# Performance work log

Measured on AMD Instinct MI355X. Metric: run time of the kernel, lower is better.

Reference implementation:

```python
import jax, jax.numpy as jnp
import numpy as np

N_POINTS = 200000   # number of voxels
N_CLUSTS = 4096     # number of clusters
P = 64              # points per cluster (regularized fixed size)
E = 32768           # number of (directed) edges


def setup_inputs() -> dict:
    key = jax.random.key(0)
    k1, k2, k3 = jax.random.split(key, 3)
    data = jax.random.normal(k1, (N_POINTS, 4), dtype=jnp.float32)
    clusts = jax.random.randint(k2, (N_CLUSTS, P), 0, N_POINTS, dtype=jnp.int64)
    edge_index = jax.random.randint(k3, (2, E), 0, N_CLUSTS, dtype=jnp.int64)
    return {"data": data, "clusts": clusts, "edge_index": edge_index}


def reference(data, clusts, edge_index):
    coords = data[:, 1:4]                      # [N, 3] voxel coordinates
    c1 = clusts[edge_index[0]]                 # [E, P] point indices of source cluster
    c2 = clusts[edge_index[1]]                 # [E, P] point indices of target cluster
    x1 = coords[c1]                            # [E, P, 3]
    x2 = coords[c2]                            # [E, P, 3]
    e, p = c1.shape
    # pairwise squared distances per edge: [E, P, P]
    d2 = jnp.sum((x1[:, :, None, :] - x2[:, None, :, :]) ** 2, axis=-1)
    imin = jnp.argmin(d2.reshape(e, p * p), axis=1)   # flat argmin of closest pair
    i1 = imin // p
    i2 = imin % p
    v1 = jnp.take_along_axis(x1, i1[:, None, None], axis=1)[:, 0, :]  # [E, 3]
    v2 = jnp.take_along_axis(x2, i2[:, None, None], axis=1)[:, 0, :]  # [E, 3]
    disp = v1 - v2                                                    # [E, 3]
    lend = jnp.linalg.norm(disp, axis=1, keepdims=True)               # [E, 1]
    safe = jnp.where(lend > 0, lend, jnp.ones_like(lend))
    disp = jnp.where(lend > 0, disp / safe, disp)                     # unit displacement
    B = (disp[:, :, None] * disp[:, None, :]).reshape(e, 9)           # outer product, flat
    return jnp.concatenate([v1, v2, disp, lend, B], axis=1)           # [E, 19]
```

## Files before the change

### kernel.cpp

```cpp
#include <hip/hip_runtime.h>

#ifndef FLT_MAX
#define FLT_MAX 3.402823466e+38f
#endif

__device__ __forceinline__ float rlanef(float v, int j) {
    return __uint_as_float(__builtin_amdgcn_readlane(__float_as_uint(v), j));
}

__device__ __forceinline__ float sel3(int i, float a, float b, float c) {
    return i == 0 ? a : (i == 1 ? b : c);
}

__device__ __forceinline__ float d2f(float ax, float ay, float az,
                                     float bx, float by, float bz) {
    const float dx = __fsub_rn(ax, bx);
    const float dy = __fsub_rn(ay, by);
    const float dz = __fsub_rn(az, bz);
    return __builtin_fmaf(dx, dx, __builtin_fmaf(dy, dy, __fmul_rn(dz, dz)));
}

__global__ __launch_bounds__(256, 8) void clustgeo_edge_kernel(
    const float* __restrict__ data,
    const int*   __restrict__ clusts,
    const int*   __restrict__ eidx,
    float*       __restrict__ out,
    int E)
{
    const int wave = threadIdx.x >> 6;
    const int lane = threadIdx.x & 63;
    const int e = blockIdx.x * 4 + wave;
    if (e >= E) return;

    __shared__ float sx2[4][3][64];

    const int a = eidx[e];
    const int b = eidx[E + e];
    const int p1 = clusts[a * 64 + lane];
    const int p2 = clusts[b * 64 + lane];
    const float4 r1 = *reinterpret_cast<const float4*>(data + (size_t)p1 * 4);
    const float4 r2 = *reinterpret_cast<const float4*>(data + (size_t)p2 * 4);
    const float x1x = r1.y, x1y = r1.z, x1z = r1.w;
    const float x2x = r2.y, x2y = r2.z, x2z = r2.w;
    sx2[wave][0][lane] = x2x;
    sx2[wave][1][lane] = x2y;
    sx2[wave][2][lane] = x2z;

    const float4* rx = reinterpret_cast<const float4*>(&sx2[wave][0][0]);
    const float4* ry = reinterpret_cast<const float4*>(&sx2[wave][1][0]);
    const float4* rz = reinterpret_cast<const float4*>(&sx2[wave][2][0]);

    float b0 = FLT_MAX, b1 = FLT_MAX, b2 = FLT_MAX, b3 = FLT_MAX;
    #pragma unroll 4
    for (int g = 0; g < 16; ++g) {
        const float4 X = rx[g];
        const float4 Y = ry[g];
        const float4 Z = rz[g];
        b0 = fminf(b0, d2f(x1x, x1y, x1z, X.x, Y.x, Z.x));
        b1 = fminf(b1, d2f(x1x, x1y, x1z, X.y, Y.y, Z.y));
        b2 = fminf(b2, d2f(x1x, x1y, x1z, X.z, Y.z, Z.z));
        b3 = fminf(b3, d2f(x1x, x1y, x1z, X.w, Y.w, Z.w));
    }
    const float rowmin = fminf(fminf(b0, b1), fminf(b2, b3));

    float bm = rowmin;
    #pragma unroll
    for (int off = 32; off; off >>= 1) bm = fminf(bm, __shfl_xor(bm, off, 64));

    const unsigned long long mi = __ballot(rowmin == bm);
    const int i1 = (int)__ffsll(mi) - 1;

    const float v1x = rlanef(x1x, i1);
    const float v1y = rlanef(x1y, i1);
    const float v1z = rlanef(x1z, i1);
    const float dj = d2f(v1x, v1y, v1z, x2x, x2y, x2z);
    const unsigned long long mj = __ballot(dj == bm);
    const int i2 = (int)__ffsll(mj) - 1;

    const float v2x = rlanef(x2x, i2);
    const float v2y = rlanef(x2y, i2);
    const float v2z = rlanef(x2z, i2);

    float dx = v1x - v2x, dy = v1y - v2y, dz = v1z - v2z;
    const float lend = sqrtf(dx * dx + dy * dy + dz * dz);
    if (lend > 0.f) { dx /= lend; dy /= lend; dz /= lend; }

    if (lane < 19) {
        float o;
        if (lane < 3)       o = sel3(lane,     v1x, v1y, v1z);
        else if (lane < 6)  o = sel3(lane - 3, v2x, v2y, v2z);
        else if (lane < 9)  o = sel3(lane - 6, dx, dy, dz);
        else if (lane == 9) o = lend;
        else {
            const int k = lane - 10;
            o = sel3(k / 3, dx, dy, dz) * sel3(k % 3, dx, dy, dz);
        }
        out[(size_t)e * 19 + lane] = o;
    }
}

extern "C" void kernel_launch(void* const* d_in, const int* in_sizes, int n_in,
                              void* d_out, int out_size, void* d_ws, size_t ws_size,
                              hipStream_t stream) {
    const float* data   = (const float*)d_in[0];
    const int*   clusts = (const int*)d_in[1];
    const int*   eidx   = (const int*)d_in[2];
    float*       out    = (float*)d_out;
    const int E = in_sizes[2] / 2;
    const int blocks = (E + 3) / 4;
    clustgeo_edge_kernel<<<blocks, 256, 0, stream>>>(data, clusts, eidx, out, E);
}
```

Measured before the change: 33.71 us.

## Process two edges per wave with half-wave split and packed fp32 math

Each 64-lane wave now handles two edges: each half-wave owns one edge, and each lane holds two source points (rows) instead of one. The pairwise distance loop uses 2-wide float vectors so the compiler can emit packed FMA/min instructions, and it reuses each LDS read across two rows. The reductions, ballots and readlanes are split per half-wave, and the grid is halved. This is meant to cut per-edge overhead from index loads, reductions and launch, at the cost of more registers per thread and more complex lane-selection logic.

```diff
diff --git a/kernel.cpp b/kernel.cpp
--- a/kernel.cpp
+++ b/kernel.cpp
@@ -4,8 +4,11 @@
 #define FLT_MAX 3.402823466e+38f
 #endif
 
-__device__ __forceinline__ float rlanef(float v, int j) {
-    return __uint_as_float(__builtin_amdgcn_readlane(__float_as_uint(v), j));
+typedef float v2f __attribute__((ext_vector_type(2)));
+typedef float v4f __attribute__((ext_vector_type(4)));
+
+__device__ __forceinline__ float rlanef(float v, int l) {
+    return __uint_as_float(__builtin_amdgcn_readlane(__float_as_uint(v), l));
 }
 
 __device__ __forceinline__ float sel3(int i, float a, float b, float c) {
@@ -29,73 +32,126 @@
 {
     const int wave = threadIdx.x >> 6;
     const int lane = threadIdx.x & 63;
-    const int e = blockIdx.x * 4 + wave;
-    if (e >= E) return;
+    const int hl   = lane & 31;
+    const bool hiH = lane >= 32;
+    const int e  = blockIdx.x * 8 + wave * 2 + (hiH ? 1 : 0);
+    const int ec = e < E ? e : (E - 1);
 
-    __shared__ float sx2[4][3][64];
+    __shared__ __align__(16) float sx2[4][2][3][64];
 
-    const int a = eidx[e];
-    const int b = eidx[E + e];
-    const int p1 = clusts[a * 64 + lane];
-    const int p2 = clusts[b * 64 + lane];
-    const float4 r1 = *reinterpret_cast<const float4*>(data + (size_t)p1 * 4);
-    const float4 r2 = *reinterpret_cast<const float4*>(data + (size_t)p2 * 4);
-    const float x1x = r1.y, x1y = r1.z, x1z = r1.w;
-    const float x2x = r2.y, x2y = r2.z, x2z = r2.w;
-    sx2[wave][0][lane] = x2x;
-    sx2[wave][1][lane] = x2y;
-    sx2[wave][2][lane] = x2z;
+    const int ca = eidx[ec];
+    const int cb = eidx[E + ec];
+    const int p1a = clusts[ca * 64 + hl];
+    const int p1b = clusts[ca * 64 + hl + 32];
+    const int p2a = clusts[cb * 64 + hl];
+    const int p2b = clusts[cb * 64 + hl + 32];
+    const float4 q1a = *reinterpret_cast<const float4*>(data + (size_t)p1a * 4);
+    const float4 q1b = *reinterpret_cast<const float4*>(data + (size_t)p1b * 4);
+    const float4 q2a = *reinterpret_cast<const float4*>(data + (size_t)p2a * 4);
+    const float4 q2b = *reinterpret_cast<const float4*>(data + (size_t)p2b * 4);
+    const float x1ax=q1a.y, x1ay=q1a.z, x1az=q1a.w;
+    const float x1bx=q1b.y, x1by=q1b.z, x1bz=q1b.w;
+    const float x2ax=q2a.y, x2ay=q2a.z, x2az=q2a.w;
+    const float x2bx=q2b.y, x2by=q2b.z, x2bz=q2b.w;
 
-    const float4* rx = reinterpret_cast<const float4*>(&sx2[wave][0][0]);
-    const float4* ry = reinterpret_cast<const float4*>(&sx2[wave][1][0]);
-    const float4* rz = reinterpret_cast<const float4*>(&sx2[wave][2][0]);
+    float* hbase = &sx2[wave][hiH ? 1 : 0][0][0];
+    hbase[hl      ] = x2ax;  hbase[hl + 32      ] = x2bx;
+    hbase[hl + 64 ] = x2ay;  hbase[hl + 32 + 64 ] = x2by;
+    hbase[hl + 128] = x2az;  hbase[hl + 32 + 128] = x2bz;
 
-    float b0 = FLT_MAX, b1 = FLT_MAX, b2 = FLT_MAX, b3 = FLT_MAX;
-    #pragma unroll 4
+    const v2f xA = {x1ax, x1ax}, yA = {x1ay, x1ay}, zA = {x1az, x1az};
+    const v2f xB = {x1bx, x1bx}, yB = {x1by, x1by}, zB = {x1bz, x1bz};
+
+    v2f r0c01 = {FLT_MAX, FLT_MAX}, r0c23 = {FLT_MAX, FLT_MAX};
+    v2f r1c01 = {FLT_MAX, FLT_MAX}, r1c23 = {FLT_MAX, FLT_MAX};
+    #pragma unroll 2
     for (int g = 0; g < 16; ++g) {
-        const float4 X = rx[g];
-        const float4 Y = ry[g];
-        const float4 Z = rz[g];
-        b0 = fminf(b0, d2f(x1x, x1y, x1z, X.x, Y.x, Z.x));
-        b1 = fminf(b1, d2f(x1x, x1y, x1z, X.y, Y.y, Z.y));
-        b2 = fminf(b2, d2f(x1x, x1y, x1z, X.z, Y.z, Z.z));
-        b3 = fminf(b3, d2f(x1x, x1y, x1z, X.w, Y.w, Z.w));
+        const v4f X = *reinterpret_cast<const v4f*>(hbase + g * 4);
+        const v4f Y = *reinterpret_cast<const v4f*>(hbase + 64 + g * 4);
+        const v4f Z = *reinterpret_cast<const v4f*>(hbase + 128 + g * 4);
+        {
+            const v2f dx = xA - X.xy, dy = yA - Y.xy, dz = zA - Z.xy;
+            r0c01 = __builtin_elementwise_min(r0c01,
+                __builtin_elementwise_fma(dx, dx, __builtin_elementwise_fma(dy, dy, dz * dz)));
+        }
+        {
+            const v2f dx = xA - X.zw, dy = yA - Y.zw, dz = zA - Z.zw;
+            r0c23 = __builtin_elementwise_min(r0c23,
+                __builtin_elementwise_fma(dx, dx, __builtin_elementwise_fma(dy, dy, dz * dz)));
+        }
+        {
+            const v2f dx = xB - X.xy, dy = yB - Y.xy, dz = zB - Z.xy;
+            r1c01 = __builtin_elementwise_min(r1c01,
+                __builtin_elementwise_fma(dx, dx, __builtin_elementwise_fma(dy, dy, dz * dz)));
+        }
+        {
+            const v2f dx = xB - X.zw, dy = yB - Y.zw, dz = zB - Z.zw;
+            r1c23 = __builtin_elementwise_min(r1c23,
+                __builtin_elementwise_fma(dx, dx, __builtin_elementwise_fma(dy, dy, dz * dz)));
+        }
     }
-    const float rowmin = fminf(fminf(b0, b1), fminf(b2, b3));
+    const float rm0 = fminf(fminf(r0c01.x, r0c01.y), fminf(r0c23.x, r0c23.y));
+    const float rm1 = fminf(fminf(r1c01.x, r1c01.y), fminf(r1c23.x, r1c23.y));
 
-    float bm = rowmin;
+    float bmv = fminf(rm0, rm1);
     #pragma unroll
-    for (int off = 32; off; off >>= 1) bm = fminf(bm, __shfl_xor(bm, off, 64));
+    for (int off = 16; off; off >>= 1) bmv = fminf(bmv, __shfl_xor(bmv, off, 64));
 
-    const unsigned long long mi = __ballot(rowmin == bm);
-    const int i1 = (int)__ffsll(mi) - 1;
+    const unsigned long long m0 = __ballot(rm0 == bmv);
+    const unsigned long long m1 = __ballot(rm1 == bmv);
+    const unsigned A0 = (unsigned)m0, A1 = (unsigned)m1;
+    const unsigned B0 = (unsigned)(m0 >> 32), B1 = (unsigned)(m1 >> 32);
+    const int i1A = A0 ? __builtin_ctz(A0) : 32 + __builtin_ctz(A1);
+    const int i1B = B0 ? __builtin_ctz(B0) : 32 + __builtin_ctz(B1);
 
-    const float v1x = rlanef(x1x, i1);
-    const float v1y = rlanef(x1y, i1);
-    const float v1z = rlanef(x1z, i1);
-    const float dj = d2f(v1x, v1y, v1z, x2x, x2y, x2z);
-    const unsigned long long mj = __ballot(dj == bm);
-    const int i2 = (int)__ffsll(mj) - 1;
+    const float v1Ax = rlanef(i1A >= 32 ? x1bx : x1ax, i1A & 31);
+    const float v1Ay = rlanef(i1A >= 32 ? x1by : x1ay, i1A & 31);
+    const float v1Az = rlanef(i1A >= 32 ? x1bz : x1az, i1A & 31);
+    const float v1Bx = rlanef(i1B >= 32 ? x1bx : x1ax, 32 + (i1B & 31));
+    const float v1By = rlanef(i1B >= 32 ? x1by : x1ay, 32 + (i1B & 31));
+    const float v1Bz = rlanef(i1B >= 32 ? x1bz : x1az, 32 + (i1B & 31));
+    const float bmA = rlanef(bmv, 0);
+    const float bmB = rlanef(bmv, 32);
 
-    const float v2x = rlanef(x2x, i2);
-    const float v2y = rlanef(x2y, i2);
-    const float v2z = rlanef(x2z, i2);
+    const float w1x = hiH ? v1Bx : v1Ax;
+    const float w1y = hiH ? v1By : v1Ay;
+    const float w1z = hiH ? v1Bz : v1Az;
+    const float bmw = hiH ? bmB : bmA;
+    const float dj0 = d2f(w1x, w1y, w1z, x2ax, x2ay, x2az);
+    const float dj1 = d2f(w1x, w1y, w1z, x2bx, x2by, x2bz);
+    const unsigned long long n0 = __ballot(dj0 == bmw);
+    const unsigned long long n1 = __ballot(dj1 == bmw);
+    const unsigned Ca0 = (unsigned)n0, Ca1 = (unsigned)n1;
+    const unsigned Cb0 = (unsigned)(n0 >> 32), Cb1 = (unsigned)(n1 >> 32);
+    const int i2A = Ca0 ? __builtin_ctz(Ca0) : 32 + __builtin_ctz(Ca1);
+    const int i2B = Cb0 ? __builtin_ctz(Cb0) : 32 + __builtin_ctz(Cb1);
 
-    float dx = v1x - v2x, dy = v1y - v2y, dz = v1z - v2z;
+    const float v2Ax = rlanef(i2A >= 32 ? x2bx : x2ax, i2A & 31);
+    const float v2Ay = rlanef(i2A >= 32 ? x2by : x2ay, i2A & 31);
+    const float v2Az = rlanef(i2A >= 32 ? x2bz : x2az, i2A & 31);
+    const float v2Bx = rlanef(i2B >= 32 ? x2bx : x2ax, 32 + (i2B & 31));
+    const float v2By = rlanef(i2B >= 32 ? x2by : x2ay, 32 + (i2B & 31));
+    const float v2Bz = rlanef(i2B >= 32 ? x2bz : x2az, 32 + (i2B & 31));
+
+    const float u2x = hiH ? v2Bx : v2Ax;
+    const float u2y = hiH ? v2By : v2Ay;
+    const float u2z = hiH ? v2Bz : v2Az;
+
+    float dx = w1x - u2x, dy = w1y - u2y, dz = w1z - u2z;
     const float lend = sqrtf(dx * dx + dy * dy + dz * dz);
     if (lend > 0.f) { dx /= lend; dy /= lend; dz /= lend; }
 
-    if (lane < 19) {
+    if (hl < 19 && e < E) {
         float o;
-        if (lane < 3)       o = sel3(lane,     v1x, v1y, v1z);
-        else if (lane < 6)  o = sel3(lane - 3, v2x, v2y, v2z);
-        else if (lane < 9)  o = sel3(lane - 6, dx, dy, dz);
-        else if (lane == 9) o = lend;
+        if (hl < 3)       o = sel3(hl,     w1x, w1y, w1z);
+        else if (hl < 6)  o = sel3(hl - 3, u2x, u2y, u2z);
+        else if (hl < 9)  o = sel3(hl - 6, dx, dy, dz);
+        else if (hl == 9) o = lend;
         else {
-            const int k = lane - 10;
+            const int k = hl - 10;
             o = sel3(k / 3, dx, dy, dz) * sel3(k % 3, dx, dy, dz);
         }
-        out[(size_t)e * 19 + lane] = o;
+        out[(size_t)e * 19 + hl] = o;
     }
 }
 
@@ -107,6 +163,6 @@
     const int*   eidx   = (const int*)d_in[2];
     float*       out    = (float*)d_out;
     const int E = in_sizes[2] / 2;
-    const int blocks = (E + 3) / 4;
+    const int blocks = (E + 7) / 8;
     clustgeo_edge_kernel<<<blocks, 256, 0, stream>>>(data, clusts, eidx, out, E);
 }
```

Result: no change. 33.25 us (-1.4%).

## Process four edges per wave with 16 lanes each and packed FP32 math

Applied to the files above, without the earlier changes.

Each wave now handles four edges instead of one. Each 16-lane group owns one edge, and every lane computes four source rows against the shared target slice. The distance loop uses 2-wide float vectors so the compiler can emit packed FP32 FMA/min, and the grid shrinks by a factor of four. The intent is to cut per-edge wave overhead and raise arithmetic throughput per lane, at the cost of more registers per thread, group-masked ballots, and a two-part output store per edge.

```diff
diff --git a/kernel.cpp b/kernel.cpp
--- a/kernel.cpp
+++ b/kernel.cpp
@@ -4,9 +4,8 @@
 #define FLT_MAX 3.402823466e+38f
 #endif
 
-__device__ __forceinline__ float rlanef(float v, int j) {
-    return __uint_as_float(__builtin_amdgcn_readlane(__float_as_uint(v), j));
-}
+typedef float v2f __attribute__((ext_vector_type(2)));
+typedef float v4f __attribute__((ext_vector_type(4)));
 
 __device__ __forceinline__ float sel3(int i, float a, float b, float c) {
     return i == 0 ? a : (i == 1 ? b : c);
@@ -20,6 +19,14 @@
     return __builtin_fmaf(dx, dx, __builtin_fmaf(dy, dy, __fmul_rn(dz, dz)));
 }
 
+__device__ __forceinline__ v2f d2p(v2f ax, v2f ay, v2f az, v2f bx, v2f by, v2f bz) {
+    const v2f dx = ax - bx, dy = ay - by, dz = az - bz;
+    return __builtin_elementwise_fma(dx, dx,
+           __builtin_elementwise_fma(dy, dy, dz * dz));
+}
+
+#define SLICE 196
+
 __global__ __launch_bounds__(256, 8) void clustgeo_edge_kernel(
     const float* __restrict__ data,
     const int*   __restrict__ clusts,
@@ -29,73 +36,121 @@
 {
     const int wave = threadIdx.x >> 6;
     const int lane = threadIdx.x & 63;
-    const int e = blockIdx.x * 4 + wave;
-    if (e >= E) return;
+    const int t    = lane & 15;
+    const int gsh  = lane & 48;
+    const int e    = blockIdx.x * 16 + wave * 4 + (lane >> 4);
+    const int ec   = e < E ? e : (E - 1);
 
-    __shared__ float sx2[4][3][64];
+    __shared__ __align__(16) float sx[4][4][SLICE];
 
-    const int a = eidx[e];
-    const int b = eidx[E + e];
-    const int p1 = clusts[a * 64 + lane];
-    const int p2 = clusts[b * 64 + lane];
-    const float4 r1 = *reinterpret_cast<const float4*>(data + (size_t)p1 * 4);
-    const float4 r2 = *reinterpret_cast<const float4*>(data + (size_t)p2 * 4);
-    const float x1x = r1.y, x1y = r1.z, x1z = r1.w;
-    const float x2x = r2.y, x2y = r2.z, x2z = r2.w;
-    sx2[wave][0][lane] = x2x;
-    sx2[wave][1][lane] = x2y;
-    sx2[wave][2][lane] = x2z;
+    const int ca = eidx[ec];
+    const int cb = eidx[E + ec];
+    const int cb64 = cb * 64 + t;
+    const int ca64 = ca * 64 + t;
 
-    const float4* rx = reinterpret_cast<const float4*>(&sx2[wave][0][0]);
-    const float4* ry = reinterpret_cast<const float4*>(&sx2[wave][1][0]);
-    const float4* rz = reinterpret_cast<const float4*>(&sx2[wave][2][0]);
+    const int p10 = clusts[ca64], p11 = clusts[ca64+16], p12 = clusts[ca64+32], p13 = clusts[ca64+48];
+    const int p20 = clusts[cb64], p21 = clusts[cb64+16], p22 = clusts[cb64+32], p23 = clusts[cb64+48];
+    const float4 q10 = *reinterpret_cast<const float4*>(data + (size_t)p10 * 4);
+    const float4 q11 = *reinterpret_cast<const float4*>(data + (size_t)p11 * 4);
+    const float4 q12 = *reinterpret_cast<const float4*>(data + (size_t)p12 * 4);
+    const float4 q13 = *reinterpret_cast<const float4*>(data + (size_t)p13 * 4);
+    const float4 q20 = *reinterpret_cast<const float4*>(data + (size_t)p20 * 4);
+    const float4 q21 = *reinterpret_cast<const float4*>(data + (size_t)p21 * 4);
+    const float4 q22 = *reinterpret_cast<const float4*>(data + (size_t)p22 * 4);
+    const float4 q23 = *reinterpret_cast<const float4*>(data + (size_t)p23 * 4);
+    const float r0x=q10.y, r0y=q10.z, r0z=q10.w;
+    const float r1x=q11.y, r1y=q11.z, r1z=q11.w;
+    const float r2x=q12.y, r2y=q12.z, r2z=q12.w;
+    const float r3x=q13.y, r3y=q13.z, r3z=q13.w;
 
-    float b0 = FLT_MAX, b1 = FLT_MAX, b2 = FLT_MAX, b3 = FLT_MAX;
+    float* slice = &sx[wave][lane >> 4][0];
+    slice[t     ] = q20.y; slice[t+16     ] = q21.y; slice[t+32     ] = q22.y; slice[t+48     ] = q23.y;
+    slice[t+64  ] = q20.z; slice[t+16+64  ] = q21.z; slice[t+32+64  ] = q22.z; slice[t+48+64  ] = q23.z;
+    slice[t+128 ] = q20.w; slice[t+16+128 ] = q21.w; slice[t+32+128 ] = q22.w; slice[t+48+128 ] = q23.w;
+
+    const v4f* SL = reinterpret_cast<const v4f*>(slice);
+
+    v2f a0 = {FLT_MAX, FLT_MAX}, a1 = {FLT_MAX, FLT_MAX};
+    v2f a2 = {FLT_MAX, FLT_MAX}, a3 = {FLT_MAX, FLT_MAX};
     #pragma unroll 4
     for (int g = 0; g < 16; ++g) {
-        const float4 X = rx[g];
-        const float4 Y = ry[g];
-        const float4 Z = rz[g];
-        b0 = fminf(b0, d2f(x1x, x1y, x1z, X.x, Y.x, Z.x));
-        b1 = fminf(b1, d2f(x1x, x1y, x1z, X.y, Y.y, Z.y));
-        b2 = fminf(b2, d2f(x1x, x1y, x1z, X.z, Y.z, Z.z));
-        b3 = fminf(b3, d2f(x1x, x1y, x1z, X.w, Y.w, Z.w));
+        const v4f X = SL[g];
+        const v4f Y = SL[16 + g];
+        const v4f Z = SL[32 + g];
+        const v2f xlo = X.xy, xhi = X.zw, ylo = Y.xy, yhi = Y.zw, zlo = Z.xy, zhi = Z.zw;
+        a0 = __builtin_elementwise_min(a0, d2p((v2f){r0x,r0x},(v2f){r0y,r0y},(v2f){r0z,r0z}, xlo, ylo, zlo));
+        a0 = __builtin_elementwise_min(a0, d2p((v2f){r0x,r0x},(v2f){r0y,r0y},(v2f){r0z,r0z}, xhi, yhi, zhi));
+        a1 = __builtin_elementwise_min(a1, d2p((v2f){r1x,r1x},(v2f){r1y,r1y},(v2f){r1z,r1z}, xlo, ylo, zlo));
+        a1 = __builtin_elementwise_min(a1, d2p((v2f){r1x,r1x},(v2f){r1y,r1y},(v2f){r1z,r1z}, xhi, yhi, zhi));
+        a2 = __builtin_elementwise_min(a2, d2p((v2f){r2x,r2x},(v2f){r2y,r2y},(v2f){r2z,r2z}, xlo, ylo, zlo));
+        a2 = __builtin_elementwise_min(a2, d2p((v2f){r2x,r2x},(v2f){r2y,r2y},(v2f){r2z,r2z}, xhi, yhi, zhi));
+        a3 = __builtin_elementwise_min(a3, d2p((v2f){r3x,r3x},(v2f){r3y,r3y},(v2f){r3z,r3z}, xlo, ylo, zlo));
+        a3 = __builtin_elementwise_min(a3, d2p((v2f){r3x,r3x},(v2f){r3y,r3y},(v2f){r3z,r3z}, xhi, yhi, zhi));
     }
-    const float rowmin = fminf(fminf(b0, b1), fminf(b2, b3));
+    const float m0 = fminf(a0.x, a0.y);
+    const float m1 = fminf(a1.x, a1.y);
+    const float m2 = fminf(a2.x, a2.y);
+    const float m3 = fminf(a3.x, a3.y);
 
-    float bm = rowmin;
+    float bmn = fminf(fminf(m0, m1), fminf(m2, m3));
     #pragma unroll
-    for (int off = 32; off; off >>= 1) bm = fminf(bm, __shfl_xor(bm, off, 64));
+    for (int off = 8; off; off >>= 1) bmn = fminf(bmn, __shfl_xor(bmn, off, 64));
 
-    const unsigned long long mi = __ballot(rowmin == bm);
-    const int i1 = (int)__ffsll(mi) - 1;
+    const unsigned g0 = (unsigned)(__ballot(m0 == bmn) >> gsh) & 0xFFFFu;
+    const unsigned g1 = (unsigned)(__ballot(m1 == bmn) >> gsh) & 0xFFFFu;
+    const unsigned g2 = (unsigned)(__ballot(m2 == bmn) >> gsh) & 0xFFFFu;
+    const unsigned g3 = (unsigned)(__ballot(m3 == bmn) >> gsh) & 0xFFFFu;
+    const int i1 = g0 ? __builtin_ctz(g0)
+                 : g1 ? 16 + __builtin_ctz(g1)
+                 : g2 ? 32 + __builtin_ctz(g2)
+                 :      48 + __builtin_ctz(g3);
 
-    const float v1x = rlanef(x1x, i1);
-    const float v1y = rlanef(x1y, i1);
-    const float v1z = rlanef(x1z, i1);
-    const float dj = d2f(v1x, v1y, v1z, x2x, x2y, x2z);
-    const unsigned long long mj = __ballot(dj == bm);
-    const int i2 = (int)__ffsll(mj) - 1;
+    const int rw = i1 >> 4;
+    const int wl = gsh + (i1 & 15);
+    const float c1x = rw == 0 ? r0x : rw == 1 ? r1x : rw == 2 ? r2x : r3x;
+    const float c1y = rw == 0 ? r0y : rw == 1 ? r1y : rw == 2 ? r2y : r3y;
+    const float c1z = rw == 0 ? r0z : rw == 1 ? r1z : rw == 2 ? r2z : r3z;
+    const float v1x = __shfl(c1x, wl, 64);
+    const float v1y = __shfl(c1y, wl, 64);
+    const float v1z = __shfl(c1z, wl, 64);
 
-    const float v2x = rlanef(x2x, i2);
-    const float v2y = rlanef(x2y, i2);
-    const float v2z = rlanef(x2z, i2);
+    const float d0 = d2f(v1x, v1y, v1z, slice[t],     slice[t+64],     slice[t+128]);
+    const float d1 = d2f(v1x, v1y, v1z, slice[t+16],  slice[t+16+64],  slice[t+16+128]);
+    const float d2_ = d2f(v1x, v1y, v1z, slice[t+32], slice[t+32+64],  slice[t+32+128]);
+    const float d3 = d2f(v1x, v1y, v1z, slice[t+48],  slice[t+48+64],  slice[t+48+128]);
+    const unsigned h0 = (unsigned)(__ballot(d0 == bmn) >> gsh) & 0xFFFFu;
+    const unsigned h1 = (unsigned)(__ballot(d1 == bmn) >> gsh) & 0xFFFFu;
+    const unsigned h2 = (unsigned)(__ballot(d2_ == bmn) >> gsh) & 0xFFFFu;
+    const unsigned h3 = (unsigned)(__ballot(d3 == bmn) >> gsh) & 0xFFFFu;
+    const int i2 = h0 ? __builtin_ctz(h0)
+                 : h1 ? 16 + __builtin_ctz(h1)
+                 : h2 ? 32 + __builtin_ctz(h2)
+                 :      48 + __builtin_ctz(h3);
+
+    const float v2x = slice[i2];
+    const float v2y = slice[i2 + 64];
+    const float v2z = slice[i2 + 128];
 
     float dx = v1x - v2x, dy = v1y - v2y, dz = v1z - v2z;
     const float lend = sqrtf(dx * dx + dy * dy + dz * dz);
     if (lend > 0.f) { dx /= lend; dy /= lend; dz /= lend; }
 
-    if (lane < 19) {
+    if (e < E) {
+        float* orow = out + (size_t)e * 19;
         float o;
-        if (lane < 3)       o = sel3(lane,     v1x, v1y, v1z);
-        else if (lane < 6)  o = sel3(lane - 3, v2x, v2y, v2z);
-        else if (lane < 9)  o = sel3(lane - 6, dx, dy, dz);
-        else if (lane == 9) o = lend;
+        if (t < 3)       o = sel3(t,     v1x, v1y, v1z);
+        else if (t < 6)  o = sel3(t - 3, v2x, v2y, v2z);
+        else if (t < 9)  o = sel3(t - 6, dx, dy, dz);
+        else if (t == 9) o = lend;
         else {
-            const int k = lane - 10;
+            const int k = t - 10;
             o = sel3(k / 3, dx, dy, dz) * sel3(k % 3, dx, dy, dz);
         }
-        out[(size_t)e * 19 + lane] = o;
+        orow[t] = o;
+        if (t < 3) {
+            const int k = t + 6;
+            orow[16 + t] = sel3(k / 3, dx, dy, dz) * sel3(k % 3, dx, dy, dz);
+        }
     }
 }
 
@@ -107,6 +162,6 @@
     const int*   eidx   = (const int*)d_in[2];
     float*       out    = (float*)d_out;
     const int E = in_sizes[2] / 2;
-    const int blocks = (E + 3) / 4;
+    const int blocks = (E + 15) / 16;
     clustgeo_edge_kernel<<<blocks, 256, 0, stream>>>(data, clusts, eidx, out, E);
 }
```

Result: slower. 76.71 us (+127.5%).
